# Kernel optimization log

Hardware: AMD Instinct MI355X
Metric: run time of the kernel (lower is better)

Reference implementation:

```python
import jax, jax.numpy as jnp
import numpy as np

jax.config.update("jax_enable_x64", True)  # original module runs the filter in float64

SR = 24000
N_CHANNELS = 64
F_MIN, F_MAX = 10.0, 100.0
R_MIN, R_MAX = 0.9999, 0.99999
BATCH, T = 8, 24000


def _make_coeffs():
    # Mirrors BidirectionalCursedIIR.__init__ buffer construction
    freqs = np.exp(np.linspace(np.log(F_MIN), np.log(F_MAX), N_CHANNELS))
    radii = np.linspace(R_MIN, R_MAX, N_CHANNELS)
    theta = 2.0 * np.pi * freqs / SR
    a0 = np.ones_like(radii)
    a1 = -2.0 * radii * np.cos(theta)
    a2 = radii ** 2
    b0 = (1.0 - radii) * 0.5
    a = np.stack([a0, a1, a2], axis=1)                      # [C, 3]
    b = np.stack([b0, np.zeros_like(b0), np.zeros_like(b0)], axis=1)  # [C, 3]
    return jnp.asarray(a, jnp.float64), jnp.asarray(b, jnp.float64)


def _iir_bank(x2d, a1, a2, b0):
    # x2d: [B, T] float64; per-channel recurrence y[n] = b0*x[n] - a1*y[n-1] - a2*y[n-2]
    B = x2d.shape[0]
    C = a1.shape[0]
    z = jnp.zeros((B, C), x2d.dtype)

    def step(carry, xt):  # xt: [B]
        y1, y2 = carry
        y = b0[None, :] * xt[:, None] - a1[None, :] * y1 - a2[None, :] * y2
        return (y, y1), y

    _, ys = jax.lax.scan(step, (z, z), jnp.moveaxis(x2d, 1, 0))  # ys: [T, B, C]
    return jnp.transpose(ys, (1, 2, 0))  # [B, C, T]


def setup_inputs() -> dict:
    key = jax.random.key(0)
    x = jax.random.normal(key, (BATCH, 1, T), dtype=jnp.float32)
    a_coeffs, b_coeffs = _make_coeffs()
    return {"x": x, "a_coeffs": a_coeffs, "b_coeffs": b_coeffs}


def reference(x, a_coeffs, b_coeffs):
    # a0 == 1 by construction, so the normalization by a0 is a no-op
    a1, a2 = a_coeffs[:, 1], a_coeffs[:, 2]
    b0 = b_coeffs[:, 0]
    xd = x[:, 0, :].astype(jnp.float64)  # [B, T]
    fwd_state = _iir_bank(xd, a1, a2, b0)                 # forward pass
    bwd_state = _iir_bank(xd[:, ::-1], a1, a2, b0)[:, :, ::-1]  # flipped pass
    return jnp.concatenate([fwd_state, bwd_state], axis=1).astype(jnp.float32)  # [B, 2C, T]
```

## Files before the change

kernel.cpp:

```cpp
#include <hip/hip_runtime.h>
#include <math.h>

#define T_LEN 24000
#define NCH   64
#define NSEQ  16
#define LCH   192
#define KCH   125
#define NBLK  (NSEQ * KCH)
#define WT    32

static_assert(KCH * LCH == T_LEN, "chunking must cover T");

struct Coeffs {
    double a1[NCH], a2[NCH], b0[NCH];
    double A00[NCH], A01[NCH], A10[NCH], A11[NCH];
};

#define ST_D2    ((size_t)NSEQ * NCH * KCH)
#define WS_NEED  (ST_D2 * sizeof(double2))

__global__ __launch_bounds__(64) void iir_endstates(
        const float* __restrict__ x, const Coeffs cf,
        double2* __restrict__ stEnd) {
    __shared__ float xs[LCH];
    const int g = blockIdx.x, k = g % KCH, s = g / KCH;
    const int bi = s >> 1, dir = s & 1, c = threadIdx.x;
    const double a1 = cf.a1[c], a2 = cf.a2[c], b0 = cf.b0[c];
    const float* xb = x + (size_t)bi * T_LEN;
    const int t0 = k * LCH;
    #pragma unroll
    for (int w = 0; w < LCH / 64; ++w) {
        const int t = t0 + w * 64 + c;
        xs[w * 64 + c] = (dir == 0) ? xb[t] : xb[T_LEN - 1 - t];
    }
    __syncthreads();
    double y1 = 0.0, y2 = 0.0;
    #pragma unroll 16
    for (int j = 0; j < LCH; ++j) {
        double y = fma(-a1, y1, fma(-a2, y2, b0 * (double)xs[j]));
        y2 = y1; y1 = y;
    }
    stEnd[((size_t)s * KCH + k) * NCH + c] = make_double2(y1, y2);
}

__global__ __launch_bounds__(64) void iir_output(
        const float* __restrict__ x, const Coeffs cf,
        const double2* __restrict__ stEnd, float* __restrict__ out) {
    __shared__ float xs[LCH];
    __shared__ __align__(16) float tile[NCH][36];
    const int g = blockIdx.x, k = g % KCH, s = g / KCH;
    const int bi = s >> 1, dir = s & 1, c = threadIdx.x;
    const double a1  = cf.a1[c],  a2  = cf.a2[c],  b0 = cf.b0[c];
    const double A00 = cf.A00[c], A01 = cf.A01[c];
    const double A10 = cf.A10[c], A11 = cf.A11[c];
    const float* xb = x + (size_t)bi * T_LEN;
    const int t0 = k * LCH;
    #pragma unroll
    for (int w = 0; w < LCH / 64; ++w) {
        const int t = t0 + w * 64 + c;
        xs[w * 64 + c] = (dir == 0) ? xb[t] : xb[T_LEN - 1 - t];
    }
    const double2* __restrict__ src = stEnd + (size_t)s * KCH * NCH;
    double in1 = 0.0, in2 = 0.0;
    #pragma unroll 8
    for (int j = 0; j < k; ++j) {
        const double2 e = src[(size_t)j * NCH + c];
        const double n1 = e.x + fma(A00, in1, A01 * in2);
        const double n2 = e.y + fma(A10, in1, A11 * in2);
        in1 = n1; in2 = n2;
    }
    __syncthreads();
    double y1 = in1, y2 = in2;
    const int rowoff = bi * 128 + (dir ? 64 : 0);
    const int lo = c & 7, hi = c >> 3;
    for (int w = 0; w < LCH / WT; ++w) {
        #pragma unroll
        for (int j4 = 0; j4 < WT / 4; ++j4) {
            float4 v;
            #pragma unroll
            for (int e = 0; e < 4; ++e) {
                double y = fma(-a1, y1,
                               fma(-a2, y2,
                                   b0 * (double)xs[w * WT + j4 * 4 + e]));
                y2 = y1; y1 = y;
                (&v.x)[dir == 0 ? e : 3 - e] = (float)y;
            }
            const int q = (dir == 0) ? j4 : (WT / 4 - 1) - j4;
            *(float4*)&tile[c][4 * q] = v;
        }
        __syncthreads();
        const int cb = (dir == 0) ? (t0 + w * WT)
                                  : (T_LEN - WT - t0 - w * WT);
        #pragma unroll
        for (int i = 0; i < 8; ++i) {
            const int r = 8 * i + hi;
            *(float4*)&out[(size_t)(rowoff + r) * T_LEN + cb + 4 * lo] =
                *(const float4*)&tile[r][4 * lo];
        }
        __syncthreads();
    }
}

__global__ __launch_bounds__(64) void iir_direct(
        const float* __restrict__ x, const Coeffs cf,
        float* __restrict__ out) {
    __shared__ float tile[NCH][65];
    const int s = blockIdx.x, bi = s >> 1, dir = s & 1, c = threadIdx.x;
    const double a1 = cf.a1[c], a2 = cf.a2[c], b0 = cf.b0[c];
    const float* xb = x + (size_t)bi * T_LEN;
    double y1 = 0.0, y2 = 0.0;
    for (int t0 = 0; t0 < T_LEN; t0 += 64) {
        #pragma unroll 8
        for (int j = 0; j < 64; ++j) {
            const int t = t0 + j;
            double xv = (dir == 0) ? (double)xb[t] : (double)xb[T_LEN - 1 - t];
            double y = fma(-a1, y1, fma(-a2, y2, b0 * xv));
            y2 = y1; y1 = y;
            tile[c][j] = (float)y;
        }
        __syncthreads();
        if (dir == 0) {
            #pragma unroll
            for (int r = 0; r < NCH; ++r)
                out[((size_t)(bi * 128 + r)) * T_LEN + (t0 + c)] = tile[r][c];
        } else {
            #pragma unroll
            for (int r = 0; r < NCH; ++r)
                out[((size_t)(bi * 128 + 64 + r)) * T_LEN +
                    (T_LEN - 1 - (t0 + c))] = tile[r][c];
        }
        __syncthreads();
    }
}

static void make_coeffs(Coeffs& cf) {
    const double l10 = log(10.0), l100 = log(100.0);
    for (int c = 0; c < NCH; ++c) {
        double lf = (c == 63) ? l100 : l10 + (double)c * ((l100 - l10) / 63.0);
        double f  = exp(lf);
        double r  = (c == 63) ? 0.99999
                              : 0.9999 + (double)c * ((0.99999 - 0.9999) / 63.0);
        double th = (2.0 * M_PI) * f / 24000.0;
        double a1 = (-2.0 * r) * cos(th), a2 = r * r, b0 = (1.0 - r) * 0.5;
        double pj1 = 1.0, pj2 = 0.0, pj3 = 0.0;
        for (int j = 0; j < LCH; ++j) {
            double p = fma(-a1, pj1, -a2 * pj2);
            pj3 = pj2; pj2 = pj1; pj1 = p;
        }
        cf.a1[c] = a1;  cf.a2[c] = a2;  cf.b0[c] = b0;
        cf.A00[c] = pj1;  cf.A01[c] = -a2 * pj2;
        cf.A10[c] = pj2;  cf.A11[c] = -a2 * pj3;
    }
}

extern "C" void kernel_launch(void* const* d_in, const int* in_sizes, int n_in,
                              void* d_out, int out_size, void* d_ws, size_t ws_size,
                              hipStream_t stream) {
    const float* x = (const float*)d_in[0];
    float* out = (float*)d_out;

    Coeffs cf;
    make_coeffs(cf);

    if (d_ws != nullptr && ws_size >= WS_NEED) {
        double2* stEnd = (double2*)d_ws;
        iir_endstates<<<NBLK, 64, 0, stream>>>(x, cf, stEnd);
        iir_output<<<NBLK, 64, 0, stream>>>(x, cf, stEnd, out);
    } else {
        iir_direct<<<NSEQ, 64, 0, stream>>>(x, cf, out);
    }
}
```

Measured before the change: 35.70 us.

## Add separate sequential carry-propagation kernel for chunk entry states

Before, every output block re-scanned all preceding chunk end-states to build its own entry state. That is O(K^2) redundant work, with late chunks doing up to 124 dependent steps. A new small kernel now runs the scan once per sequence, 16 blocks of 64 threads, writes entry states to a second workspace buffer, and the output kernel just loads its entry state. This adds a kernel launch and a serial 125-step stage with very little parallelism, and it needs twice the workspace; it falls back to the old path if the workspace is smaller.

```diff
diff --git a/kernel.cpp b/kernel.cpp
--- a/kernel.cpp
+++ b/kernel.cpp
@@ -8,16 +8,19 @@
 #define KCH   125
 #define NBLK  (NSEQ * KCH)
 #define WT    32
+#define KB2   25
 
 static_assert(KCH * LCH == T_LEN, "chunking must cover T");
+static_assert(KCH % KB2 == 0, "P2 batches must cover KCH");
 
 struct Coeffs {
     double a1[NCH], a2[NCH], b0[NCH];
     double A00[NCH], A01[NCH], A10[NCH], A11[NCH];
 };
 
-#define ST_D2    ((size_t)NSEQ * NCH * KCH)
-#define WS_NEED  (ST_D2 * sizeof(double2))
+#define ST_D2     ((size_t)NSEQ * NCH * KCH)
+#define WS_FULL   (2 * ST_D2 * sizeof(double2))
+#define WS_MID    (ST_D2 * sizeof(double2))
 
 __global__ __launch_bounds__(64) void iir_endstates(
         const float* __restrict__ x, const Coeffs cf,
@@ -43,7 +46,79 @@
     stEnd[((size_t)s * KCH + k) * NCH + c] = make_double2(y1, y2);
 }
 
+__global__ __launch_bounds__(64) void iir_entries(
+        const Coeffs cf, const double2* __restrict__ stEnd,
+        double2* __restrict__ stEntry) {
+    const int s = blockIdx.x, c = threadIdx.x;
+    const double A00 = cf.A00[c], A01 = cf.A01[c];
+    const double A10 = cf.A10[c], A11 = cf.A11[c];
+    const double2* __restrict__ src = stEnd + (size_t)s * KCH * NCH;
+    double2* __restrict__ dst = stEntry + (size_t)s * KCH * NCH;
+    double in1 = 0.0, in2 = 0.0;
+    for (int kb = 0; kb < KCH; kb += KB2) {
+        double2 e[KB2];
+        #pragma unroll
+        for (int j = 0; j < KB2; ++j)
+            e[j] = src[(size_t)(kb + j) * NCH + c];
+        #pragma unroll
+        for (int j = 0; j < KB2; ++j) {
+            dst[(size_t)(kb + j) * NCH + c] = make_double2(in1, in2);
+            const double n1 = e[j].x + fma(A00, in1, A01 * in2);
+            const double n2 = e[j].y + fma(A10, in1, A11 * in2);
+            in1 = n1; in2 = n2;
+        }
+    }
+}
+
 __global__ __launch_bounds__(64) void iir_output(
+        const float* __restrict__ x, const Coeffs cf,
+        const double2* __restrict__ stEntry, float* __restrict__ out) {
+    __shared__ float xs[LCH];
+    __shared__ __align__(16) float tile[NCH][36];
+    const int g = blockIdx.x, k = g % KCH, s = g / KCH;
+    const int bi = s >> 1, dir = s & 1, c = threadIdx.x;
+    const double a1 = cf.a1[c], a2 = cf.a2[c], b0 = cf.b0[c];
+    const double2 ent = stEntry[((size_t)s * KCH + k) * NCH + c];
+    const float* xb = x + (size_t)bi * T_LEN;
+    const int t0 = k * LCH;
+    #pragma unroll
+    for (int w = 0; w < LCH / 64; ++w) {
+        const int t = t0 + w * 64 + c;
+        xs[w * 64 + c] = (dir == 0) ? xb[t] : xb[T_LEN - 1 - t];
+    }
+    __syncthreads();
+    double y1 = ent.x, y2 = ent.y;
+    const int rowoff = bi * 128 + (dir ? 64 : 0);
+    const int lo = c & 7, hi = c >> 3;
+    for (int w = 0; w < LCH / WT; ++w) {
+        #pragma unroll
+        for (int j4 = 0; j4 < WT / 4; ++j4) {
+            float4 v;
+            #pragma unroll
+            for (int e = 0; e < 4; ++e) {
+                double y = fma(-a1, y1,
+                               fma(-a2, y2,
+                                   b0 * (double)xs[w * WT + j4 * 4 + e]));
+                y2 = y1; y1 = y;
+                (&v.x)[dir == 0 ? e : 3 - e] = (float)y;
+            }
+            const int q = (dir == 0) ? j4 : (WT / 4 - 1) - j4;
+            *(float4*)&tile[c][4 * q] = v;
+        }
+        __syncthreads();
+        const int cb = (dir == 0) ? (t0 + w * WT)
+                                  : (T_LEN - WT - t0 - w * WT);
+        #pragma unroll
+        for (int i = 0; i < 8; ++i) {
+            const int r = 8 * i + hi;
+            *(float4*)&out[(size_t)(rowoff + r) * T_LEN + cb + 4 * lo] =
+                *(const float4*)&tile[r][4 * lo];
+        }
+        __syncthreads();
+    }
+}
+
+__global__ __launch_bounds__(64) void iir_output_scan(
         const float* __restrict__ x, const Coeffs cf,
         const double2* __restrict__ stEnd, float* __restrict__ out) {
     __shared__ float xs[LCH];
@@ -162,10 +237,16 @@
     Coeffs cf;
     make_coeffs(cf);
 
-    if (d_ws != nullptr && ws_size >= WS_NEED) {
+    if (d_ws != nullptr && ws_size >= WS_FULL) {
+        double2* stEnd = (double2*)d_ws;
+        double2* stEntry = stEnd + ST_D2;
+        iir_endstates<<<NBLK, 64, 0, stream>>>(x, cf, stEnd);
+        iir_entries<<<NSEQ, 64, 0, stream>>>(cf, stEnd, stEntry);
+        iir_output<<<NBLK, 64, 0, stream>>>(x, cf, stEntry, out);
+    } else if (d_ws != nullptr && ws_size >= WS_MID) {
         double2* stEnd = (double2*)d_ws;
         iir_endstates<<<NBLK, 64, 0, stream>>>(x, cf, stEnd);
-        iir_output<<<NBLK, 64, 0, stream>>>(x, cf, stEnd, out);
+        iir_output_scan<<<NBLK, 64, 0, stream>>>(x, cf, stEnd, out);
     } else {
         iir_direct<<<NSEQ, 64, 0, stream>>>(x, cf, out);
     }
```

Result: no change. 35.20 us (-1.4%).
